# Optimization experiments

Hardware: AMD Instinct MI355X
Metric: run time of the kernel (lower is better)

Reference implementation:

```python
import jax, jax.numpy as jnp
import numpy as np

B, S, H, D = 256, 512, 256, 512  # batch, n_seq, n_hid, n_dim
LN_EPS = 1e-5


def _xavier(key, fan_out, fan_in):
    lim = (6.0 / (fan_in + fan_out)) ** 0.5
    return jax.random.uniform(key, (fan_out, fan_in), jnp.float32, -lim, lim)


def setup_inputs() -> dict:
    key = jax.random.key(0)
    ks = jax.random.split(key, 10)
    x = jax.random.normal(ks[0], (B, S, D), jnp.float32)
    k_w = _xavier(ks[1], H, D)
    q_w = _xavier(ks[2], H, D)
    v_w = _xavier(ks[3], H, D)
    lb = 1.0 / (D ** 0.5)
    k_b = jax.random.uniform(ks[4], (H,), jnp.float32, -lb, lb)
    q_b = jax.random.uniform(ks[5], (H,), jnp.float32, -lb, lb)
    v_b = jax.random.uniform(ks[6], (H,), jnp.float32, -lb, lb)
    attn_bias = jax.random.normal(ks[7], (S, H), jnp.float32)
    ln_g = jnp.ones((H,), jnp.float32)
    ln_b = jnp.zeros((H,), jnp.float32)
    lo = 1.0 / ((S * H) ** 0.5)
    out_w = jax.random.uniform(ks[8], (D, S * H), jnp.float32, -lo, lo)
    out_b = jax.random.uniform(ks[9], (D,), jnp.float32, -lo, lo)
    return {"x": x, "k_w": k_w, "k_b": k_b, "q_w": q_w, "q_b": q_b,
            "v_w": v_w, "v_b": v_b, "attn_bias": attn_bias,
            "ln_g": ln_g, "ln_b": ln_b, "out_w": out_w, "out_b": out_b}


def reference(x, k_w, k_b, q_w, q_b, v_w, v_b, attn_bias, ln_g, ln_b, out_w, out_b):
    # projections: [B,S,D] -> [B,S,H]
    k = jnp.einsum('bsd,hd->bsh', x, k_w) + k_b
    q = jnp.einsum('bsd,hd->bsh', x, q_w) + q_b
    v = jnp.einsum('bsd,hd->bsh', x, v_w) + v_b
    # scores = k^T q, scaled by BATCH size^-0.5 (faithful to v.shape[0]**-0.5)
    scale = x.shape[0] ** (-0.5)
    scores = jnp.einsum('bsh,bsg->bhg', k, q) * scale  # [B,H,H]
    weight = jax.nn.softmax(scores, axis=1)
    out = jnp.einsum('bsh,bhg->bsg', v, weight)  # [B,S,H]
    out = out + attn_bias
    # LayerNorm over last dim
    mu = out.mean(-1, keepdims=True)
    var = out.var(-1, keepdims=True)
    out = (out - mu) * jax.lax.rsqrt(var + LN_EPS) * ln_g + ln_b
    # dropout is identity in eval mode; exact (erf) GELU matches torch default
    out = jax.nn.gelu(out, approximate=False)
    out = out.reshape(out.shape[0], S * H)
    out = out @ out_w.T + out_b  # [B,D]
    return out[:, None, :]  # [B,1,D]
```

## Files before the change

kernel.cpp:

```cpp
#include <hip/hip_runtime.h>
#include <hip/hip_bf16.h>
#include <math.h>

#define B_ 256
#define S_ 512
#define H_ 256
#define D_ 512

typedef __bf16 bf16;
typedef __bf16 bf16x8 __attribute__((ext_vector_type(8)));
typedef float  f32x4  __attribute__((ext_vector_type(4)));
typedef unsigned short u16x8 __attribute__((ext_vector_type(8)));
typedef unsigned short u16x4 __attribute__((ext_vector_type(4)));

#define MFMA(a, b, c) __builtin_amdgcn_mfma_f32_16x16x32_bf16((a), (b), (c), 0, 0, 0)

__device__ __forceinline__ int swz(int row, int kbyte) {
  return (row * 128 + kbyte) ^ ((row & 7) << 4);
}
__device__ __forceinline__ unsigned short bfbits(float f) {
  bf16 h = (bf16)f;
  union { bf16 b; unsigned short u; } c; c.b = h; return c.u;
}
__device__ __forceinline__ bf16x8 cvt8(const float* __restrict__ p) {
  f32x4 a = *(const f32x4*)p;
  f32x4 b = *(const f32x4*)(p + 4);
  bf16x8 r;
  r[0] = (bf16)a[0]; r[1] = (bf16)a[1]; r[2] = (bf16)a[2]; r[3] = (bf16)a[3];
  r[4] = (bf16)b[0]; r[5] = (bf16)b[1]; r[6] = (bf16)b[2]; r[7] = (bf16)b[3];
  return r;
}
__device__ __forceinline__ void gload16(const unsigned short* g, unsigned char* l) {
  __builtin_amdgcn_global_load_lds(
      (const __attribute__((address_space(1))) unsigned int*)g,
      (__attribute__((address_space(3))) unsigned int*)l, 16, 0, 0);
}

__global__ __launch_bounds__(256) void k_convw(
    const float* __restrict__ kw, const float* __restrict__ qw,
    const float* __restrict__ vw, unsigned short* __restrict__ wc)
{
  const int r = blockIdx.x;
  const float* src = (r < 256) ? kw + (size_t)r * 512
                   : (r < 512) ? qw + (size_t)(r - 256) * 512
                               : vw + (size_t)(r - 512) * 512;
  const int c = threadIdx.x * 2;
  wc[(size_t)r * 512 + c]     = bfbits(src[c]);
  wc[(size_t)r * 512 + c + 1] = bfbits(src[c + 1]);
}

__global__ __launch_bounds__(256) void k_proj2(
    const float* __restrict__ x,
    const unsigned short* __restrict__ wc,
    const float* __restrict__ kbi, const float* __restrict__ qbi,
    const float* __restrict__ vbi,
    unsigned short* __restrict__ k_t, unsigned short* __restrict__ q_t,
    unsigned short* __restrict__ v_o, int nwg)
{
  __shared__ __align__(16) unsigned char sA[16384];
  __shared__ __align__(16) unsigned char sB[16384];

  const int o = blockIdx.x;
  const int cpx = nwg >> 3;
  const int a = (o & 7) * cpx + (o >> 3);
  const int mt = a / 6;
  const int nb = a - mt * 6;
  const int m0 = mt * 128;
  const int n0 = nb * 128;
  const int region = nb >> 1;
  const int h0 = (nb & 1) * 128;
  const float* __restrict__ Bi = (region == 0) ? kbi : (region == 1) ? qbi : vbi;

  const int tid = threadIdx.x;
  const int lane = tid & 63;
  const int wid = tid >> 6;
  const int wm = wid >> 1;
  const int wn = wid & 1;
  const int l15 = lane & 15;

  f32x4 acc[4][4];
#pragma unroll
  for (int i = 0; i < 4; ++i)
#pragma unroll
    for (int j = 0; j < 4; ++j) acc[i][j] = (f32x4){0.f, 0.f, 0.f, 0.f};

  const int lr = lane >> 3;
  const int lk = (lane & 7) << 3;

  for (int kt = 0; kt < 8; ++kt) {
    if (kt) __syncthreads();
#pragma unroll
    for (int i = 0; i < 4; ++i) {
      int c = tid + i * 256;
      int row = c >> 3, kc = (c & 7) * 8;
      *(bf16x8*)(sA + swz(row, kc * 2)) =
          cvt8(x + (size_t)(m0 + row) * D_ + kt * 64 + kc);
    }
#pragma unroll
    for (int i = 0; i < 4; ++i) {
      const int chunk = wid * 4 + i;
      const int row = chunk * 8 + lr;
      gload16(wc + (size_t)(n0 + row) * 512 + kt * 64 + lk, sB + chunk * 1024);
    }
    __syncthreads();
#pragma unroll
    for (int ks = 0; ks < 2; ++ks) {
      const int kb2 = ks * 64 + ((lane >> 4) << 4);
      bf16x8 av[4], bv[4];
#pragma unroll
      for (int f = 0; f < 4; ++f)
        av[f] = *(const bf16x8*)(sA + swz(wm * 64 + f * 16 + l15, kb2));
#pragma unroll
      for (int f = 0; f < 4; ++f)
        bv[f] = *(const bf16x8*)(sB + (wn * 64 + f * 16 + l15) * 128 + kb2);
#pragma unroll
      for (int fm = 0; fm < 4; ++fm)
#pragma unroll
        for (int fn = 0; fn < 4; ++fn)
          acc[fm][fn] = MFMA(av[fm], bv[fn], acc[fm][fn]);
    }
  }

  const int b = m0 >> 9;
  const int sbase = m0 & 511;
  const int r4 = (lane >> 4) * 4;
#pragma unroll
  for (int fn = 0; fn < 4; ++fn) {
    const int hcol = h0 + wn * 64 + fn * 16 + l15;
    const float bias = Bi[hcol];
#pragma unroll
    for (int fm = 0; fm < 4; ++fm) {
      const int s = sbase + wm * 64 + fm * 16 + r4;
      if (region < 2) {
        unsigned short* dst = ((region == 0) ? k_t : q_t) +
                              (size_t)b * (H_ * S_) + (size_t)hcol * S_ + s;
        u16x4 ov;
#pragma unroll
        for (int j = 0; j < 4; ++j) ov[j] = bfbits(acc[fm][fn][j] + bias);
        *(u16x4*)dst = ov;
      } else {
#pragma unroll
        for (int j = 0; j < 4; ++j)
          v_o[(size_t)b * (S_ * H_) + (size_t)(s + j) * H_ + hcol] =
              bfbits(acc[fm][fn][j] + bias);
      }
    }
  }
}

__global__ __launch_bounds__(1024, 4) void k_attn(
    const unsigned short* __restrict__ k_t,
    const unsigned short* __restrict__ q_t,
    const unsigned short* __restrict__ v_o,
    const float* __restrict__ attn_bias,
    const float* __restrict__ lng, const float* __restrict__ lnb,
    unsigned short* __restrict__ act)
{
  __shared__ __align__(16) unsigned char sm[147456];
  unsigned char* sP = sm;
  unsigned char* sK = sm;
  unsigned char* sQ = sm + 32768;
  unsigned char* sV = sm + 131072;
  float* redm = (float*)(sm + 131072);
  float* reds = (float*)(sm + 131072 + 4096);
  float* lbuf = (float*)(sm + 131072);

  const int tid = threadIdx.x;
  const int lane = tid & 63;
  const int wid = tid >> 6;
  const int l15 = lane & 15;
  const int l16 = lane >> 4;
  const int b = blockIdx.x;
  const int wh = wid >> 2;
  const int wq = wid & 3;

  const unsigned short* __restrict__ Kb = k_t + (size_t)b * (H_ * S_);
  const unsigned short* __restrict__ Qb = q_t + (size_t)b * (H_ * S_);
  const unsigned short* __restrict__ Vb = v_o + (size_t)b * (S_ * H_);

  const int srow8 = lane >> 3;
  const int scol16 = (lane & 7) ^ srow8;

  f32x4 acc1[4][4];
#pragma unroll
  for (int i = 0; i < 4; ++i)
#pragma unroll
    for (int j = 0; j < 4; ++j) acc1[i][j] = (f32x4){0.f, 0.f, 0.f, 0.f};

  for (int kt = 0; kt < 8; ++kt) {
    if (kt) __syncthreads();
#pragma unroll
    for (int i = 0; i < 2; ++i) {
      const int cb = wid * 2 + i;
      const int row = cb * 8 + srow8;
      gload16(Kb + (size_t)row * S_ + kt * 64 + scol16 * 8, sK + cb * 1024);
      gload16(Qb + (size_t)row * S_ + kt * 64 + scol16 * 8, sQ + cb * 1024);
    }
    __syncthreads();
#pragma unroll
    for (int ks = 0; ks < 2; ++ks) {
      const int kb2 = ks * 64 + l16 * 16;
      bf16x8 av[4], bv[4];
#pragma unroll
      for (int f = 0; f < 4; ++f)
        av[f] = *(const bf16x8*)(sK + swz(wh * 64 + f * 16 + l15, kb2));
#pragma unroll
      for (int f = 0; f < 4; ++f)
        bv[f] = *(const bf16x8*)(sQ + swz(wq * 64 + f * 16 + l15, kb2));
#pragma unroll
      for (int fm = 0; fm < 4; ++fm)
#pragma unroll
        for (int fn = 0; fn < 4; ++fn)
          acc1[fm][fn] = MFMA(av[fm], bv[fn], acc1[fm][fn]);
    }
  }

  float cmax[4] = {-3.0e38f, -3.0e38f, -3.0e38f, -3.0e38f};
#pragma unroll
  for (int fm = 0; fm < 4; ++fm)
#pragma unroll
    for (int fn = 0; fn < 4; ++fn)
#pragma unroll
      for (int j = 0; j < 4; ++j) {
        acc1[fm][fn][j] *= 0.0625f;
        cmax[fn] = fmaxf(cmax[fn], acc1[fm][fn][j]);
      }
#pragma unroll
  for (int fn = 0; fn < 4; ++fn) {
    cmax[fn] = fmaxf(cmax[fn], __shfl_xor(cmax[fn], 16));
    cmax[fn] = fmaxf(cmax[fn], __shfl_xor(cmax[fn], 32));
  }
  if (lane < 16) {
#pragma unroll
    for (int fn = 0; fn < 4; ++fn)
      redm[wh * 256 + wq * 64 + fn * 16 + lane] = cmax[fn];
  }
  __syncthreads();
  float gmax[4];
#pragma unroll
  for (int fn = 0; fn < 4; ++fn) {
    const int c = wq * 64 + fn * 16 + l15;
    gmax[fn] = fmaxf(fmaxf(redm[c], redm[256 + c]),
                     fmaxf(redm[512 + c], redm[768 + c]));
  }
  float csum[4] = {0.f, 0.f, 0.f, 0.f};
#pragma unroll
  for (int fm = 0; fm < 4; ++fm)
#pragma unroll
    for (int fn = 0; fn < 4; ++fn)
#pragma unroll
      for (int j = 0; j < 4; ++j) {
        float p = __expf(acc1[fm][fn][j] - gmax[fn]);
        acc1[fm][fn][j] = p;
        csum[fn] += p;
      }
#pragma unroll
  for (int fn = 0; fn < 4; ++fn) {
    csum[fn] += __shfl_xor(csum[fn], 16);
    csum[fn] += __shfl_xor(csum[fn], 32);
  }
  if (lane < 16) {
#pragma unroll
    for (int fn = 0; fn < 4; ++fn)
      reds[wh * 256 + wq * 64 + fn * 16 + lane] = csum[fn];
  }
  __syncthreads();
  float gi[4];
#pragma unroll
  for (int fn = 0; fn < 4; ++fn) {
    const int c = wq * 64 + fn * 16 + l15;
    gi[fn] = 1.0f / (reds[c] + reds[256 + c] + reds[512 + c] + reds[768 + c]);
  }

#pragma unroll
  for (int fn = 0; fn < 4; ++fn) {
    const int g = wq * 64 + fn * 16 + l15;
#pragma unroll
    for (int fm = 0; fm < 4; ++fm) {
      const int h0 = wh * 64 + fm * 16 + l16 * 4;
      u16x4 pv;
#pragma unroll
      for (int j = 0; j < 4; ++j) pv[j] = bfbits(acc1[fm][fn][j] * gi[fn]);
      *(u16x4*)(sP + ((g * 512 + h0 * 2) ^ ((g & 7) << 4))) = pv;
    }
  }

  const int vrow = tid >> 2;
  const int vcol16 = (tid & 3) ^ ((vrow >> 1) & 3);

  for (int so = 0; so < 2; ++so) {
    f32x4 acc2[4][4];
#pragma unroll
    for (int i = 0; i < 4; ++i)
#pragma unroll
      for (int j = 0; j < 4; ++j) acc2[i][j] = (f32x4){0.f, 0.f, 0.f, 0.f};

    for (int kh = 0; kh < 8; ++kh) {
      __syncthreads();
      gload16(Vb + (size_t)(so * 256 + vrow) * H_ + kh * 32 + vcol16 * 8,
              sV + wid * 1024);
      __syncthreads();
      bf16x8 av[4], bv[4];
#pragma unroll
      for (int f = 0; f < 4; ++f) {
        const int rl = wh * 64 + f * 16 + l15;
        av[f] = *(const bf16x8*)(sV + rl * 64 + ((l16 ^ ((rl >> 1) & 3)) << 4));
      }
#pragma unroll
      for (int fn = 0; fn < 4; ++fn) {
        const int g = wq * 64 + fn * 16 + l15;
        bv[fn] = *(const bf16x8*)(
            sP + ((g * 512 + kh * 64 + l16 * 16) ^ ((g & 7) << 4)));
      }
#pragma unroll
      for (int f = 0; f < 4; ++f)
#pragma unroll
        for (int fn = 0; fn < 4; ++fn)
          acc2[f][fn] = MFMA(av[f], bv[fn], acc2[f][fn]);
    }
    __syncthreads();

#pragma unroll
    for (int f = 0; f < 4; ++f) {
#pragma unroll
      for (int j = 0; j < 4; ++j) {
        const int rloc = wh * 64 + f * 16 + l16 * 4 + j;
        const int s = so * 256 + rloc;
        float ps = 0.f, psq = 0.f;
#pragma unroll
        for (int fn = 0; fn < 4; ++fn) {
          const int g = wq * 64 + fn * 16 + l15;
          float vv = acc2[f][fn][j] + attn_bias[(size_t)s * H_ + g];
          acc2[f][fn][j] = vv;
          ps += vv; psq += vv * vv;
        }
        ps += __shfl_xor(ps, 1);  psq += __shfl_xor(psq, 1);
        ps += __shfl_xor(ps, 2);  psq += __shfl_xor(psq, 2);
        ps += __shfl_xor(ps, 4);  psq += __shfl_xor(psq, 4);
        ps += __shfl_xor(ps, 8);  psq += __shfl_xor(psq, 8);
        if (l15 == 0) {
          lbuf[wq * 256 + rloc] = ps;
          lbuf[1024 + wq * 256 + rloc] = psq;
        }
      }
    }
    __syncthreads();
#pragma unroll
    for (int f = 0; f < 4; ++f) {
#pragma unroll
      for (int j = 0; j < 4; ++j) {
        const int rloc = wh * 64 + f * 16 + l16 * 4 + j;
        const int s = so * 256 + rloc;
        float sum = lbuf[rloc] + lbuf[256 + rloc] +
                    lbuf[512 + rloc] + lbuf[768 + rloc];
        float sq  = lbuf[1024 + rloc] + lbuf[1280 + rloc] +
                    lbuf[1536 + rloc] + lbuf[1792 + rloc];
        float mu = sum * (1.f / H_);
        float var = sq * (1.f / H_) - mu * mu;
        float rstd = rsqrtf(var + 1e-5f);
#pragma unroll
        for (int fn = 0; fn < 4; ++fn) {
          const int g = wq * 64 + fn * 16 + l15;
          float xv = (acc2[f][fn][j] - mu) * rstd * lng[g] + lnb[g];
          float y = 0.5f * xv * (1.f + erff(xv * 0.70710678118654752f));
          act[(size_t)b * (S_ * H_) + (size_t)s * H_ + g] = bfbits(y);
        }
      }
    }
  }
}

__global__ __launch_bounds__(512) void k_final(
    const unsigned short* __restrict__ act,
    const float* __restrict__ ow,
    float* __restrict__ partial)
{
  __shared__ __align__(16) unsigned char sA[256 * 128];
  __shared__ __align__(16) unsigned char sB[64 * 128];

  const int tid = threadIdx.x;
  const int lane = tid & 63;
  const int wid = tid >> 6;
  const int wm = wid >> 1;
  const int wn = wid & 1;
  const int n0 = blockIdx.x * 64;
  const size_t k0 = (size_t)blockIdx.y * 4096;

  f32x4 acc[4][2];
#pragma unroll
  for (int i = 0; i < 4; ++i)
#pragma unroll
    for (int j = 0; j < 2; ++j) acc[i][j] = (f32x4){0.f, 0.f, 0.f, 0.f};

  for (int kt = 0; kt < 64; ++kt) {
    const size_t kb = k0 + kt * 64;
    __syncthreads();
#pragma unroll
    for (int i = 0; i < 4; ++i) {
      int c = tid + i * 512;
      int row = c >> 3, kc = (c & 7) * 8;
      *(u16x8*)(sA + swz(row, kc * 2)) =
          *(const u16x8*)(act + (size_t)row * 131072 + kb + kc);
    }
    {
      int row = tid >> 3, kc = (tid & 7) * 8;
      *(bf16x8*)(sB + swz(row, kc * 2)) =
          cvt8(ow + (size_t)(n0 + row) * 131072 + kb + kc);
    }
    __syncthreads();
#pragma unroll
    for (int ks = 0; ks < 2; ++ks) {
      const int kbyte = ks * 64 + (lane >> 4) * 16;
      bf16x8 av[4], bv[2];
#pragma unroll
      for (int f = 0; f < 4; ++f)
        av[f] = *(const bf16x8*)(sA + swz(wm * 64 + f * 16 + (lane & 15), kbyte));
#pragma unroll
      for (int f = 0; f < 2; ++f)
        bv[f] = *(const bf16x8*)(sB + swz(wn * 32 + f * 16 + (lane & 15), kbyte));
#pragma unroll
      for (int fm = 0; fm < 4; ++fm)
#pragma unroll
        for (int fn = 0; fn < 2; ++fn)
          acc[fm][fn] = MFMA(av[fm], bv[fn], acc[fm][fn]);
    }
  }

  float* __restrict__ P = partial + (size_t)blockIdx.y * (256 * 512);
  const int r4 = (lane >> 4) * 4;
#pragma unroll
  for (int fn = 0; fn < 2; ++fn) {
    int col = n0 + wn * 32 + fn * 16 + (lane & 15);
#pragma unroll
    for (int fm = 0; fm < 4; ++fm) {
      int mb = wm * 64 + fm * 16 + r4;
#pragma unroll
      for (int j = 0; j < 4; ++j)
        P[(size_t)(mb + j) * 512 + col] = acc[fm][fn][j];
    }
  }
}

__global__ __launch_bounds__(256) void k_reduce(
    const float* __restrict__ partial,
    const float* __restrict__ ob,
    float* __restrict__ out)
{
  const int i4 = blockIdx.x * 256 + threadIdx.x;
  f32x4 s = *(const f32x4*)(ob + ((i4 & 127) << 2));
#pragma unroll
  for (int ks = 0; ks < 32; ++ks)
    s += *(const f32x4*)(partial + (size_t)ks * 131072 + (size_t)i4 * 4);
  *(f32x4*)(out + (size_t)i4 * 4) = s;
}

extern "C" void kernel_launch(void* const* d_in, const int* in_sizes, int n_in,
                              void* d_out, int out_size, void* d_ws, size_t ws_size,
                              hipStream_t stream) {
  const float* x         = (const float*)d_in[0];
  const float* k_w       = (const float*)d_in[1];
  const float* k_b       = (const float*)d_in[2];
  const float* q_w       = (const float*)d_in[3];
  const float* q_b       = (const float*)d_in[4];
  const float* v_w       = (const float*)d_in[5];
  const float* v_b       = (const float*)d_in[6];
  const float* attn_bias = (const float*)d_in[7];
  const float* ln_g      = (const float*)d_in[8];
  const float* ln_b      = (const float*)d_in[9];
  const float* out_w     = (const float*)d_in[10];
  const float* out_b     = (const float*)d_in[11];
  float* out = (float*)d_out;

  char* ws = (char*)d_ws;
  unsigned short* k_t = (unsigned short*)(ws);
  unsigned short* q_t = (unsigned short*)(ws + 67108864);
  unsigned short* v_o = (unsigned short*)(ws + 134217728);
  unsigned short* wc  = (unsigned short*)(ws + 201326592);
  unsigned short* act = k_t;
  float* partial      = (float*)(ws + 67108864);

  k_convw<<<dim3(768), dim3(256), 0, stream>>>(k_w, q_w, v_w, wc);

  const int nwg = 6144;
  k_proj2<<<dim3(nwg), dim3(256), 0, stream>>>(
      x, wc, k_b, q_b, v_b, k_t, q_t, v_o, nwg);

  k_attn<<<dim3(256), dim3(1024), 0, stream>>>(
      k_t, q_t, v_o, attn_bias, ln_g, ln_b, act);

  k_final<<<dim3(8, 32), dim3(512), 0, stream>>>(act, out_w, partial);
  k_reduce<<<dim3(128), dim3(256), 0, stream>>>(partial, out_b, out);
}
```

Measured before the change: 476.1 us.

## Double-buffer global-to-LDS loads in projection and attention GEMM loops

The projection kernel now prefetches the next K-tile of x into registers and the next weight tile into a second LDS buffer while the current tile is computed, using explicit waitcnt and raw barriers. The attention kernel gets the same double-buffering for the K/Q score loop and for the V staging loop, and shared memory grows to hold both buffers. The goal is to hide global memory latency behind MFMA work and drop one barrier per iteration. In exchange, LDS use and register pressure go up, and hand-written vmcnt counts must match the number of outstanding loads.

Result: slower. 519.4 us (+9.1%).

```diff
diff --git a/kernel.cpp b/kernel.cpp
--- a/kernel.cpp
+++ b/kernel.cpp
@@ -49,7 +49,7 @@
   wc[(size_t)r * 512 + c + 1] = bfbits(src[c + 1]);
 }
 
-__global__ __launch_bounds__(256) void k_proj2(
+__global__ __launch_bounds__(256) void k_proj3(
     const float* __restrict__ x,
     const unsigned short* __restrict__ wc,
     const float* __restrict__ kbi, const float* __restrict__ qbi,
@@ -58,7 +58,7 @@
     unsigned short* __restrict__ v_o, int nwg)
 {
   __shared__ __align__(16) unsigned char sA[16384];
-  __shared__ __align__(16) unsigned char sB[16384];
+  __shared__ __align__(16) unsigned char sB[32768];
 
   const int o = blockIdx.x;
   const int cpx = nwg >> 3;
@@ -77,32 +77,61 @@
   const int wm = wid >> 1;
   const int wn = wid & 1;
   const int l15 = lane & 15;
-
-  f32x4 acc[4][4];
-#pragma unroll
-  for (int i = 0; i < 4; ++i)
-#pragma unroll
-    for (int j = 0; j < 4; ++j) acc[i][j] = (f32x4){0.f, 0.f, 0.f, 0.f};
-
   const int lr = lane >> 3;
   const int lk = (lane & 7) << 3;
 
-  for (int kt = 0; kt < 8; ++kt) {
-    if (kt) __syncthreads();
+  f32x4 acc[4][4];
+#pragma unroll
+  for (int i = 0; i < 4; ++i)
+#pragma unroll
+    for (int j = 0; j < 4; ++j) acc[i][j] = (f32x4){0.f, 0.f, 0.f, 0.f};
+
+  auto issueB = [&](int kt, int buf) {
+#pragma unroll
+    for (int i = 0; i < 4; ++i) {
+      const int chunk = wid * 4 + i;
+      const int row = chunk * 8 + lr;
+      gload16(wc + (size_t)(n0 + row) * 512 + kt * 64 + lk,
+              sB + buf * 16384 + chunk * 1024);
+    }
+  };
+
+  f32x4 pa[4], pb[4];
+  auto loadA = [&](int kt) {
 #pragma unroll
     for (int i = 0; i < 4; ++i) {
       int c = tid + i * 256;
       int row = c >> 3, kc = (c & 7) * 8;
-      *(bf16x8*)(sA + swz(row, kc * 2)) =
-          cvt8(x + (size_t)(m0 + row) * D_ + kt * 64 + kc);
-    }
+      const float* p = x + (size_t)(m0 + row) * D_ + kt * 64 + kc;
+      pa[i] = *(const f32x4*)p;
+      pb[i] = *(const f32x4*)(p + 4);
+    }
+  };
+
+  loadA(0);
+  issueB(0, 0);
+
+  for (int kt = 0; kt < 8; ++kt) {
+    const int cur = kt & 1;
+    __builtin_amdgcn_s_barrier();
+    __builtin_amdgcn_sched_barrier(0);
 #pragma unroll
     for (int i = 0; i < 4; ++i) {
-      const int chunk = wid * 4 + i;
-      const int row = chunk * 8 + lr;
-      gload16(wc + (size_t)(n0 + row) * 512 + kt * 64 + lk, sB + chunk * 1024);
-    }
-    __syncthreads();
+      int c = tid + i * 256;
+      int row = c >> 3, kc = (c & 7) * 8;
+      bf16x8 r;
+      r[0] = (bf16)pa[i][0]; r[1] = (bf16)pa[i][1];
+      r[2] = (bf16)pa[i][2]; r[3] = (bf16)pa[i][3];
+      r[4] = (bf16)pb[i][0]; r[5] = (bf16)pb[i][1];
+      r[6] = (bf16)pb[i][2]; r[7] = (bf16)pb[i][3];
+      *(bf16x8*)(sA + swz(row, kc * 2)) = r;
+    }
+    if (kt < 7) issueB(kt + 1, cur ^ 1);
+    if (kt < 7) asm volatile("s_waitcnt vmcnt(4) lgkmcnt(0)" ::: "memory");
+    else        asm volatile("s_waitcnt vmcnt(0) lgkmcnt(0)" ::: "memory");
+    __builtin_amdgcn_s_barrier();
+    __builtin_amdgcn_sched_barrier(0);
+    if (kt < 7) loadA(kt + 1);
 #pragma unroll
     for (int ks = 0; ks < 2; ++ks) {
       const int kb2 = ks * 64 + ((lane >> 4) << 4);
@@ -112,13 +141,14 @@
         av[f] = *(const bf16x8*)(sA + swz(wm * 64 + f * 16 + l15, kb2));
 #pragma unroll
       for (int f = 0; f < 4; ++f)
-        bv[f] = *(const bf16x8*)(sB + (wn * 64 + f * 16 + l15) * 128 + kb2);
+        bv[f] = *(const bf16x8*)(sB + cur * 16384 + (wn * 64 + f * 16 + l15) * 128 + kb2);
 #pragma unroll
       for (int fm = 0; fm < 4; ++fm)
 #pragma unroll
         for (int fn = 0; fn < 4; ++fn)
           acc[fm][fn] = MFMA(av[fm], bv[fn], acc[fm][fn]);
     }
+    __builtin_amdgcn_sched_barrier(0);
   }
 
   const int b = m0 >> 9;
@@ -156,14 +186,11 @@
     const float* __restrict__ lng, const float* __restrict__ lnb,
     unsigned short* __restrict__ act)
 {
-  __shared__ __align__(16) unsigned char sm[147456];
+  __shared__ __align__(16) unsigned char sm[163840];
   unsigned char* sP = sm;
-  unsigned char* sK = sm;
-  unsigned char* sQ = sm + 32768;
-  unsigned char* sV = sm + 131072;
   float* redm = (float*)(sm + 131072);
   float* reds = (float*)(sm + 131072 + 4096);
-  float* lbuf = (float*)(sm + 131072);
+  float* lbuf = (float*)(sm + 147456);
 
   const int tid = threadIdx.x;
   const int lane = tid & 63;
@@ -181,22 +208,34 @@
   const int srow8 = lane >> 3;
   const int scol16 = (lane & 7) ^ srow8;
 
-  f32x4 acc1[4][4];
-#pragma unroll
-  for (int i = 0; i < 4; ++i)
-#pragma unroll
-    for (int j = 0; j < 4; ++j) acc1[i][j] = (f32x4){0.f, 0.f, 0.f, 0.f};
-
-  for (int kt = 0; kt < 8; ++kt) {
-    if (kt) __syncthreads();
+  auto stage1 = [&](int t, int buf) {
 #pragma unroll
     for (int i = 0; i < 2; ++i) {
       const int cb = wid * 2 + i;
       const int row = cb * 8 + srow8;
-      gload16(Kb + (size_t)row * S_ + kt * 64 + scol16 * 8, sK + cb * 1024);
-      gload16(Qb + (size_t)row * S_ + kt * 64 + scol16 * 8, sQ + cb * 1024);
-    }
-    __syncthreads();
+      gload16(Kb + (size_t)row * S_ + t * 64 + scol16 * 8,
+              sm + buf * 65536 + cb * 1024);
+      gload16(Qb + (size_t)row * S_ + t * 64 + scol16 * 8,
+              sm + buf * 65536 + 32768 + cb * 1024);
+    }
+  };
+
+  f32x4 acc1[4][4];
+#pragma unroll
+  for (int i = 0; i < 4; ++i)
+#pragma unroll
+    for (int j = 0; j < 4; ++j) acc1[i][j] = (f32x4){0.f, 0.f, 0.f, 0.f};
+
+  stage1(0, 0);
+  for (int t = 0; t < 8; ++t) {
+    const int cur = t & 1;
+    if (t < 7) stage1(t + 1, cur ^ 1);
+    if (t < 7) asm volatile("s_waitcnt vmcnt(4)" ::: "memory");
+    else       asm volatile("s_waitcnt vmcnt(0)" ::: "memory");
+    __builtin_amdgcn_s_barrier();
+    __builtin_amdgcn_sched_barrier(0);
+    const unsigned char* sK = sm + cur * 65536;
+    const unsigned char* sQ = sK + 32768;
 #pragma unroll
     for (int ks = 0; ks < 2; ++ks) {
       const int kb2 = ks * 64 + l16 * 16;
@@ -213,6 +252,8 @@
         for (int fn = 0; fn < 4; ++fn)
           acc1[fm][fn] = MFMA(av[fm], bv[fn], acc1[fm][fn]);
     }
+    __builtin_amdgcn_sched_barrier(0);
+    __builtin_amdgcn_s_barrier();
   }
 
   float cmax[4] = {-3.0e38f, -3.0e38f, -3.0e38f, -3.0e38f};
@@ -284,88 +325,104 @@
       *(u16x4*)(sP + ((g * 512 + h0 * 2) ^ ((g & 7) << 4))) = pv;
     }
   }
+  __syncthreads();
 
   const int vrow = tid >> 2;
   const int vcol16 = (tid & 3) ^ ((vrow >> 1) & 3);
 
-  for (int so = 0; so < 2; ++so) {
-    f32x4 acc2[4][4];
-#pragma unroll
-    for (int i = 0; i < 4; ++i)
-#pragma unroll
-      for (int j = 0; j < 4; ++j) acc2[i][j] = (f32x4){0.f, 0.f, 0.f, 0.f};
-
-    for (int kh = 0; kh < 8; ++kh) {
+  auto stageV = [&](int t) {
+    const int so_ = t >> 3, kh_ = t & 7;
+    gload16(Vb + (size_t)(so_ * 256 + vrow) * H_ + kh_ * 32 + vcol16 * 8,
+            sm + 131072 + (t & 1) * 16384 + wid * 1024);
+  };
+
+  f32x4 acc2[4][4];
+  stageV(0);
+  for (int t = 0; t < 16; ++t) {
+    const int so = t >> 3, kh = t & 7, cur = t & 1;
+    if (kh == 0) {
+#pragma unroll
+      for (int i = 0; i < 4; ++i)
+#pragma unroll
+        for (int j = 0; j < 4; ++j) acc2[i][j] = (f32x4){0.f, 0.f, 0.f, 0.f};
+    }
+    if (t < 15) stageV(t + 1);
+    if (t < 15) asm volatile("s_waitcnt vmcnt(1)" ::: "memory");
+    else        asm volatile("s_waitcnt vmcnt(0)" ::: "memory");
+    __builtin_amdgcn_s_barrier();
+    __builtin_amdgcn_sched_barrier(0);
+    const unsigned char* sV = sm + 131072 + cur * 16384;
+    bf16x8 av[4], bv[4];
+#pragma unroll
+    for (int f = 0; f < 4; ++f) {
+      const int rl = wh * 64 + f * 16 + l15;
+      av[f] = *(const bf16x8*)(sV + rl * 64 + ((l16 ^ ((rl >> 1) & 3)) << 4));
+    }
+#pragma unroll
+    for (int fn = 0; fn < 4; ++fn) {
+      const int g = wq * 64 + fn * 16 + l15;
+      bv[fn] = *(const bf16x8*)(
+          sP + ((g * 512 + kh * 64 + l16 * 16) ^ ((g & 7) << 4)));
+    }
+#pragma unroll
+    for (int f = 0; f < 4; ++f)
+#pragma unroll
+      for (int fn = 0; fn < 4; ++fn)
+        acc2[f][fn] = MFMA(av[f], bv[fn], acc2[f][fn]);
+    __builtin_amdgcn_sched_barrier(0);
+
+    if (kh == 7) {
       __syncthreads();
-      gload16(Vb + (size_t)(so * 256 + vrow) * H_ + kh * 32 + vcol16 * 8,
-              sV + wid * 1024);
-      __syncthreads();
-      bf16x8 av[4], bv[4];
 #pragma unroll
       for (int f = 0; f < 4; ++f) {
-        const int rl = wh * 64 + f * 16 + l15;
-        av[f] = *(const bf16x8*)(sV + rl * 64 + ((l16 ^ ((rl >> 1) & 3)) << 4));
-      }
-#pragma unroll
-      for (int fn = 0; fn < 4; ++fn) {
-        const int g = wq * 64 + fn * 16 + l15;
-        bv[fn] = *(const bf16x8*)(
-            sP + ((g * 512 + kh * 64 + l16 * 16) ^ ((g & 7) << 4)));
-      }
-#pragma unroll
-      for (int f = 0; f < 4; ++f)
-#pragma unroll
-        for (int fn = 0; fn < 4; ++fn)
-          acc2[f][fn] = MFMA(av[f], bv[fn], acc2[f][fn]);
-    }
-    __syncthreads();
-
-#pragma unroll
-    for (int f = 0; f < 4; ++f) {
-#pragma unroll
-      for (int j = 0; j < 4; ++j) {
-        const int rloc = wh * 64 + f * 16 + l16 * 4 + j;
-        const int s = so * 256 + rloc;
-        float ps = 0.f, psq = 0.f;
-#pragma unroll
-        for (int fn = 0; fn < 4; ++fn) {
-          const int g = wq * 64 + fn * 16 + l15;
-          float vv = acc2[f][fn][j] + attn_bias[(size_t)s * H_ + g];
-          acc2[f][fn][j] = vv;
-          ps += vv; psq += vv * vv;
-        }
-        ps += __shfl_xor(ps, 1);  psq += __shfl_xor(psq, 1);
-        ps += __shfl_xor(ps, 2);  psq += __shfl_xor(psq, 2);
-        ps += __shfl_xor(ps, 4);  psq += __shfl_xor(psq, 4);
-        ps += __shfl_xor(ps, 8);  psq += __shfl_xor(psq, 8);
-        if (l15 == 0) {
-          lbuf[wq * 256 + rloc] = ps;
-          lbuf[1024 + wq * 256 + rloc] = psq;
+#pragma unroll
+        for (int j = 0; j < 4; ++j) {
+          const int rloc = wh * 64 + f * 16 + l16 * 4 + j;
+          const int s = so * 256 + rloc;
+          float ps = 0.f, psq = 0.f;
+#pragma unroll
+          for (int fn = 0; fn < 4; ++fn) {
+            const int g = wq * 64 + fn * 16 + l15;
+            float vv = acc2[f][fn][j] + attn_bias[(size_t)s * H_ + g];
+            acc2[f][fn][j] = vv;
+            ps += vv; psq += vv * vv;
+          }
+          ps += __shfl_xor(ps, 1);  psq += __shfl_xor(psq, 1);
+          ps += __shfl_xor(ps, 2);  psq += __shfl_xor(psq, 2);
+          ps += __shfl_xor(ps, 4);  psq += __shfl_xor(psq, 4);
+          ps += __shfl_xor(ps, 8);  psq += __shfl_xor(psq, 8);
+          if (l15 == 0) {
+            lbuf[wq * 256 + rloc] = ps;
+            lbuf[1024 + wq * 256 + rloc] = psq;
+          }
         }
       }
-    }
-    __syncthreads();
-#pragma unroll
-    for (int f = 0; f < 4; ++f) {
-#pragma unroll
-      for (int j = 0; j < 4; ++j) {
-        const int rloc = wh * 64 + f * 16 + l16 * 4 + j;
-        const int s = so * 256 + rloc;
-        float sum = lbuf[rloc] + lbuf[256 + rloc] +
-                    lbuf[512 + rloc] + lbuf[768 + rloc];
-        float sq  = lbuf[1024 + rloc] + lbuf[1280 + rloc] +
-                    lbuf[1536 + rloc] + lbuf[1792 + rloc];
-        float mu = sum * (1.f / H_);
-        float var = sq * (1.f / H_) - mu * mu;
-        float rstd = rsqrtf(var + 1e-5f);
-#pragma unroll
-        for (int fn = 0; fn < 4; ++fn) {
-          const int g = wq * 64 + fn * 16 + l15;
-          float xv = (acc2[f][fn][j] - mu) * rstd * lng[g] + lnb[g];
-          float y = 0.5f * xv * (1.f + erff(xv * 0.70710678118654752f));
-          act[(size_t)b * (S_ * H_) + (size_t)s * H_ + g] = bfbits(y);
+      __syncthreads();
+#pragma unroll
+      for (int f = 0; f < 4; ++f) {
+#pragma unroll
+        for (int j = 0; j < 4; ++j) {
+          const int rloc = wh * 64 + f * 16 + l16 * 4 + j;
+          const int s = so * 256 + rloc;
+          float sum = lbuf[rloc] + lbuf[256 + rloc] +
+                      lbuf[512 + rloc] + lbuf[768 + rloc];
+          float sq  = lbuf[1024 + rloc] + lbuf[1280 + rloc] +
+                      lbuf[1536 + rloc] + lbuf[1792 + rloc];
+          float mu = sum * (1.f / H_);
+          float var = sq * (1.f / H_) - mu * mu;
+          float rstd = rsqrtf(var + 1e-5f);
+#pragma unroll
+          for (int fn = 0; fn < 4; ++fn) {
+            const int g = wq * 64 + fn * 16 + l15;
+            float xv = (acc2[f][fn][j] - mu) * rstd * lng[g] + lnb[g];
+            float y = 0.5f * xv * (1.f + erff(xv * 0.70710678118654752f));
+            act[(size_t)b * (S_ * H_) + (size_t)s * H_ + g] = bfbits(y);
+          }
         }
       }
+      __syncthreads();
+    } else {
+      __builtin_amdgcn_s_barrier();
     }
   }
 }
@@ -482,7 +539,7 @@
   k_convw<<<dim3(768), dim3(256), 0, stream>>>(k_w, q_w, v_w, wc);
 
   const int nwg = 6144;
-  k_proj2<<<dim3(nwg), dim3(256), 0, stream>>>(
+  k_proj3<<<dim3(nwg), dim3(256), 0, stream>>>(
       x, wc, k_b, q_b, v_b, k_t, q_t, v_o, nwg);
 
   k_attn<<<dim3(256), dim3(1024), 0, stream>>>(
```
